# Kernel optimization log

Hardware: AMD Instinct MI355X
Metric: run time of the kernel (lower is better)

## Reference

```python
import jax, jax.numpy as jnp
import numpy as np
from jax import lax

BN_EPS = 1e-5
K_TOP = 2


def _conv_bn_relu_pool(x, w, b, g, beta, mean, var):
    # x: [B,C,H,W], w: [O,I,3,3]; SAME conv -> eval BN -> ReLU -> 2x2 maxpool
    y = lax.conv_general_dilated(x, w, (1, 1), 'SAME',
                                 dimension_numbers=('NCHW', 'OIHW', 'NCHW'))
    y = y + b[None, :, None, None]
    inv = g / jnp.sqrt(var + BN_EPS)
    y = (y - mean[None, :, None, None]) * inv[None, :, None, None] + beta[None, :, None, None]
    y = jax.nn.relu(y)
    return lax.reduce_window(y, -jnp.inf, lax.max, (1, 1, 2, 2), (1, 1, 2, 2), 'VALID')


def setup_inputs() -> dict:
    key = jax.random.key(0)
    ks = jax.random.split(key, 12)
    B, F_DIM, H_DIM, OUT, E = 4096, 128, 64, 10, 8
    d = {}
    d['x'] = jax.random.normal(ks[0], (B, 3, 32, 32), dtype=jnp.float32)
    # conv stacks
    def conv_block(k, cin, cout, i):
        kk = jax.random.split(k, 2)
        d[f'conv{i}_w'] = jax.random.normal(kk[0], (cout, cin, 3, 3), dtype=jnp.float32) * (1.0 / np.sqrt(cin * 9))
        d[f'conv{i}_b'] = jnp.zeros((cout,), dtype=jnp.float32)
        d[f'bn{i}_g'] = jnp.ones((cout,), dtype=jnp.float32)
        d[f'bn{i}_b'] = jnp.zeros((cout,), dtype=jnp.float32)
        d[f'bn{i}_m'] = jax.random.normal(kk[1], (cout,), dtype=jnp.float32) * 0.1
        d[f'bn{i}_v'] = jnp.ones((cout,), dtype=jnp.float32)
    conv_block(ks[1], 3, 32, 1)
    conv_block(ks[2], 32, 64, 2)
    conv_block(ks[3], 64, 128, 3)
    # experts (stacked): MLPHead Linear(128,64) -> ReLU -> Linear(64,10)
    d['w1'] = jax.random.normal(ks[4], (E, F_DIM, H_DIM), dtype=jnp.float32) * (1.0 / np.sqrt(F_DIM))
    d['b1'] = jnp.zeros((E, H_DIM), dtype=jnp.float32)
    d['w2'] = jax.random.normal(ks[5], (E, H_DIM, OUT), dtype=jnp.float32) * (1.0 / np.sqrt(H_DIM))
    d['b2'] = jnp.zeros((E, OUT), dtype=jnp.float32)
    # top-k gate: Linear(128, 8)
    d['gate_w'] = jax.random.normal(ks[6], (F_DIM, E), dtype=jnp.float32) * (1.0 / np.sqrt(F_DIM))
    d['gate_b'] = jnp.zeros((E,), dtype=jnp.float32)
    return d


def reference(x, conv1_w, conv1_b, bn1_g, bn1_b, bn1_m, bn1_v,
              conv2_w, conv2_b, bn2_g, bn2_b, bn2_m, bn2_v,
              conv3_w, conv3_b, bn3_g, bn3_b, bn3_m, bn3_v,
              w1, b1, w2, b2, gate_w, gate_b):
    # Backbone: 3x32x32 -> 128 (eval-mode BN, dropout identity)
    h = _conv_bn_relu_pool(x, conv1_w, conv1_b, bn1_g, bn1_b, bn1_m, bn1_v)  # [B,32,16,16]
    h = _conv_bn_relu_pool(h, conv2_w, conv2_b, bn2_g, bn2_b, bn2_m, bn2_v)  # [B,64,8,8]
    h = _conv_bn_relu_pool(h, conv3_w, conv3_b, bn3_g, bn3_b, bn3_m, bn3_v)  # [B,128,4,4]
    feat = jnp.mean(h, axis=(2, 3))  # AdaptiveAvgPool2d(1) + Flatten -> [B,128]

    # Top-k gate: logits -> top-k -> softmax over selected -> scatter to [B,E]
    logits = feat @ gate_w + gate_b                     # [B,E]
    vals, idx = lax.top_k(logits, K_TOP)                # [B,k]
    wk = jax.nn.softmax(vals, axis=-1)                  # [B,k]
    B, E = logits.shape
    weights = jnp.zeros((B, E), dtype=logits.dtype)
    weights = weights.at[jnp.arange(B)[:, None], idx].set(wk)

    # Dense expert MLPs (as in source), gate-weighted sum
    he = jax.nn.relu(jnp.einsum('bf,efh->beh', feat, w1) + b1[None])  # [B,E,H]
    oe = jnp.einsum('beh,eho->beo', he, w2) + b2[None]                # [B,E,O]
    return jnp.einsum('be,beo->bo', weights, oe)                      # [B,O]
```

## Files before the change

### kernel.cpp

```cpp
#include <hip/hip_runtime.h>
#include <math.h>

typedef __attribute__((ext_vector_type(8))) short short8;
typedef __attribute__((ext_vector_type(4))) float f32x4;
typedef __attribute__((ext_vector_type(16))) float f32x16;
#define MFMA16 __builtin_amdgcn_mfma_f32_16x16x32_bf16
#define MFMA32 __builtin_amdgcn_mfma_f32_32x32x16_bf16

#define BN_EPS 1e-5f

static const size_t W1C2_OFF = 0;
static const size_t W2C2_OFF = 1024;
static const size_t W3C2_OFF = 19456;
static const size_t B1_OFF   = 93184;
static const size_t B2_OFF   = 93216;
static const size_t B3_OFF   = 93280;

__device__ inline unsigned short rneb(float x) {
    unsigned u = __float_as_uint(x);
    return (unsigned short)((u + 0x7FFFu + ((u >> 16) & 1u)) >> 16);
}
__device__ inline float b2f(unsigned short h) {
    return __uint_as_float(((unsigned)h) << 16);
}

__global__ __launch_bounds__(256) void k_prep(
    const float* __restrict__ c1w, const float* __restrict__ c2w, const float* __restrict__ c3w,
    const float* __restrict__ c1b, const float* __restrict__ g1, const float* __restrict__ be1,
    const float* __restrict__ m1, const float* __restrict__ v1,
    const float* __restrict__ c2b, const float* __restrict__ g2, const float* __restrict__ be2,
    const float* __restrict__ m2, const float* __restrict__ v2,
    const float* __restrict__ c3b, const float* __restrict__ g3, const float* __restrict__ be3,
    const float* __restrict__ m3, const float* __restrict__ v3,
    unsigned short* __restrict__ w1c2, unsigned short* __restrict__ w2c2,
    unsigned short* __restrict__ w3c2,
    float* __restrict__ b1c, float* __restrict__ b2c, float* __restrict__ b3c)
{
    int i = blockIdx.x * 256 + threadIdx.x;
    if (i < 2048) {
        int e = i & 7, p = (i >> 3) & 1, kc = (i >> 4) & 3, ol = (i >> 6) & 15, n = i >> 10;
        int o = n * 16 + ol, k = kc * 8 + e;
        float s = g1[o] * rsqrtf(v1[o] + BN_EPS);
        float wv = (k < 27) ? c1w[o * 27 + k] * s : 0.f;
        unsigned short h = rneb(wv);
        w1c2[i] = p ? rneb(wv - b2f(h)) : h;
        return;
    }
    i -= 2048;
    if (i < 36864) {
        int e = i & 7, p = (i >> 3) & 1, kh = (i >> 4) & 1, col = (i >> 5) & 31;
        int nt = (i >> 10) & 1, ks = (i >> 11) & 1, tap = i >> 12;
        int o = nt * 32 + col, ci = ks * 16 + kh * 8 + e;
        float s = g2[o] * rsqrtf(v2[o] + BN_EPS);
        float wv = c2w[o * 288 + ci * 9 + tap] * s;
        unsigned short h = rneb(wv);
        w2c2[i] = p ? rneb(wv - b2f(h)) : h;
        return;
    }
    i -= 36864;
    if (i < 147456) {
        int e = i & 7, p = (i >> 3) & 1, kh = (i >> 4) & 1, col = (i >> 5) & 31;
        int nf = (i >> 10) & 3, ks = (i >> 12) & 3, tap = i >> 14;
        int o = nf * 32 + col, ci = ks * 16 + kh * 8 + e;
        float sc = g3[o] * rsqrtf(v3[o] + BN_EPS);
        float wv = c3w[o * 576 + ci * 9 + tap] * sc;
        unsigned short h = rneb(wv);
        w3c2[i] = p ? rneb(wv - b2f(h)) : h;
        return;
    }
    i -= 147456;
    if (i < 32) { float s = g1[i]*rsqrtf(v1[i]+BN_EPS); b1c[i] = (c1b[i]-m1[i])*s + be1[i]; return; }
    i -= 32;
    if (i < 64) { float s = g2[i]*rsqrtf(v2[i]+BN_EPS); b2c[i] = (c2b[i]-m2[i])*s + be2[i]; return; }
    i -= 64;
    if (i < 128) { float s = g3[i]*rsqrtf(v3[i]+BN_EPS); b3c[i] = (c3b[i]-m3[i])*s + be3[i]; return; }
}

__global__ __launch_bounds__(512, 4) void k_fused(
    const float* __restrict__ x,
    const unsigned short* __restrict__ w1c2,
    const unsigned short* __restrict__ w2c2,
    const unsigned short* __restrict__ w3c2,
    const float* __restrict__ b1c, const float* __restrict__ b2c, const float* __restrict__ b3c,
    const float* __restrict__ w1e, const float* __restrict__ b1e,
    const float* __restrict__ w2e, const float* __restrict__ b2e,
    const float* __restrict__ gw, const float* __restrict__ gb,
    float* __restrict__ out)
{
    __shared__ __align__(16) unsigned short R1[20736];
    __shared__ __align__(16) unsigned int   R2x[3074];
    float* sFeatP = (float*)R2x;
    float* sPart  = (float*)R2x + 256;
    float* sOutB  = (float*)R2x + 768;

    const int b = blockIdx.x, t = threadIdx.x;
    const int lane = t & 63, w = t >> 6;
    const int l15 = lane & 15, lg = lane >> 4;
    const int4 z4 = {0, 0, 0, 0};

    {
        const float* xb = x + (size_t)b * 3072;
        for (int i = t; i < 3072; i += 512) {
            float v = xb[i];
            unsigned short h = rneb(v);
            unsigned short lo = rneb(v - b2f(h));
            R2x[i] = ((unsigned)h << 16) | lo;
        }
        if (t == 0) R2x[3072] = 0;
        for (int hh = t; hh < 272; hh += 512) {
            int pr = hh >> 2, kc = hh & 3;
            int py, px;
            if (pr < 36) { py = (pr < 18) ? 0 : 17; px = (pr < 18) ? pr : pr - 18; }
            else { int r = pr - 36; py = 1 + (r >> 1); px = (r & 1) ? 17 : 0; }
            int ei = ((py * 4 + kc) * 18 + px) * 8;
            *(int4*)(R1 + ei) = z4;
            *(int4*)(R1 + 10368 + ei) = z4;
        }
    }
    __syncthreads();

    {
        short8 b1h[2], b1l[2];
#pragma unroll
        for (int n = 0; n < 2; n++) {
            const short8* bp = (const short8*)(w1c2 + 16 * ((n * 16 + l15) * 4 + lg));
            b1h[n] = bp[0]; b1l[n] = bp[1];
        }
        int dyE[8], dxE[8], cbE[8];
#pragma unroll
        for (int e = 0; e < 8; e++) {
            int k = lg * 8 + e;
            if (k < 27) { int ci = k / 9, tp = k - ci * 9;
                          dyE[e] = tp / 3 - 1; dxE[e] = tp % 3 - 1; cbE[e] = ci << 10; }
            else { dyE[e] = -1000; dxE[e] = 0; cbE[e] = 0; }
        }
        float bia[2] = { b1c[l15], b1c[16 + l15] };
#pragma unroll 1
        for (int q = 0; q < 2; q++) {
            int m0 = 8 * w + 4 * q;
            f32x4 acc[4][2];
#pragma unroll
            for (int mi = 0; mi < 4; mi++)
#pragma unroll
                for (int n = 0; n < 2; n++) acc[mi][n] = (f32x4)0.f;
#pragma unroll
            for (int mi = 0; mi < 4; mi++) {
                int pos = 16 * (m0 + mi) + l15, py = pos >> 5, px = pos & 31;
                short8 ah, al;
#pragma unroll
                for (int e = 0; e < 8; e++) {
                    int yy = py + dyE[e], xv = px + dxE[e];
                    int idx = cbE[e] + (yy << 5) + xv;
                    bool ok = ((unsigned)yy < 32u) && ((unsigned)xv < 32u);
                    unsigned u = R2x[ok ? idx : 3072];
                    ah[e] = (short)(u >> 16);
                    al[e] = (short)(u & 0xFFFFu);
                }
#pragma unroll
                for (int n = 0; n < 2; n++) {
                    acc[mi][n] = MFMA16(ah, b1h[n], acc[mi][n], 0, 0, 0);
                    acc[mi][n] = MFMA16(ah, b1l[n], acc[mi][n], 0, 0, 0);
                    acc[mi][n] = MFMA16(al, b1h[n], acc[mi][n], 0, 0, 0);
                }
            }
            int PY = 2 * w + q;
#pragma unroll
            for (int n = 0; n < 2; n++) {
                int o = n * 16 + l15;
#pragma unroll
                for (int h = 0; h < 2; h++)
#pragma unroll
                for (int jp = 0; jp < 2; jp++) {
                    float v00 = fmaxf(acc[h][n][2*jp]     + bia[n], 0.f);
                    float v01 = fmaxf(acc[h][n][2*jp + 1] + bia[n], 0.f);
                    float v10 = fmaxf(acc[h+2][n][2*jp]     + bia[n], 0.f);
                    float v11 = fmaxf(acc[h+2][n][2*jp + 1] + bia[n], 0.f);
                    float pm = fmaxf(fmaxf(v00, v01), fmaxf(v10, v11));
                    int PX = h * 8 + lg * 2 + jp;
                    unsigned short ph = rneb(pm), pl = rneb(pm - b2f(ph));
                    int ei = (((PY + 1) * 4 + (o >> 3)) * 18 + (PX + 1)) * 8 + (o & 7);
                    R1[ei] = ph; R1[10368 + ei] = pl;
                }
            }
        }
    }
    __syncthreads();

    {
        const int nt = w & 1, wm = w >> 1;
        const int r = lane & 31, kh = lane >> 5;
        f32x16 acc2A = (f32x16)0.f, acc2B = (f32x16)0.f;
        const unsigned short* wb = w2c2 + ((size_t)(nt * 32 + r) * 2 + kh) * 16;
        const int pyb0 = 2 * (2 * wm)     + (r >> 4);
        const int pyb1 = 2 * (2 * wm + 1) + (r >> 4);
        const int pxb = r & 15;
#pragma unroll
        for (int u = 0; u < 18; u++) {
            const int tap_ = u >> 1, ks_ = u & 1;
            const int dy_ = tap_ / 3, dx_ = tap_ - 3 * dy_;
            const int kc_ = ks_ * 2 + kh;
            const int co_ = (kc_ * 18 + pxb + dx_) * 8;
            const short8* bp = (const short8*)(wb + u * 2048);
            short8 bh = bp[0], bl = bp[1];
            {
                int ea_ = (pyb0 + dy_) * 576 + co_;
                short8 ah_ = *(const short8*)(R1 + ea_);
                short8 al_ = *(const short8*)(R1 + 10368 + ea_);
                acc2A = MFMA32(ah_, bh, acc2A, 0, 0, 0);
                acc2A = MFMA32(ah_, bl, acc2A, 0, 0, 0);
                acc2A = MFMA32(al_, bh, acc2A, 0, 0, 0);
            }
            {
                int ea_ = (pyb1 + dy_) * 576 + co_;
                short8 ah_ = *(const short8*)(R1 + ea_);
                short8 al_ = *(const short8*)(R1 + 10368 + ea_);
                acc2B = MFMA32(ah_, bh, acc2B, 0, 0, 0);
                acc2B = MFMA32(ah_, bl, acc2B, 0, 0, 0);
                acc2B = MFMA32(al_, bh, acc2B, 0, 0, 0);
            }
        }
        __syncthreads();
        for (int hh = t; hh < 288; hh += 512) {
            int pr = hh >> 3, kc = hh & 7;
            int py, px;
            if (pr < 20) { py = (pr < 10) ? 0 : 9; px = (pr < 10) ? pr : pr - 10; }
            else { int rr = pr - 20; py = 1 + (rr >> 1); px = (rr & 1) ? 9 : 0; }
            int ei = ((py * 8 + kc) * 11 + px) * 8;
            *(int4*)(R1 + ei) = z4;
            *(int4*)(R1 + 7040 + ei) = z4;
        }
        {
            int oc = nt * 32 + r;
            float bia = b2c[oc];
#define EPI2(ACC, MT) { \
            _Pragma("unroll") for (int g = 0; g < 4; g++) { \
                float v0 = fmaxf(ACC[2*g]     + bia, 0.f); \
                float v1 = fmaxf(ACC[2*g + 1] + bia, 0.f); \
                float v2 = fmaxf(ACC[2*g + 8] + bia, 0.f); \
                float v3 = fmaxf(ACC[2*g + 9] + bia, 0.f); \
                float pm = fmaxf(fmaxf(v0, v1), fmaxf(v2, v3)); \
                int PX = (g & 1) + (g >> 1) * 4 + kh * 2; \
                int ei = ((((MT) + 1) * 8 + (oc >> 3)) * 11 + (PX + 1)) * 8 + (oc & 7); \
                unsigned short ph = rneb(pm); \
                R1[ei] = ph; R1[7040 + ei] = rneb(pm - b2f(ph)); } }
            EPI2(acc2A, 2 * wm);
            EPI2(acc2B, 2 * wm + 1);
        }
    }
    __syncthreads();

    {
        const int mt = w >> 2, nf = w & 3;
        const int r = lane & 31, kh = lane >> 5;
        f32x16 acc3a = (f32x16)0.f, acc3b = (f32x16)0.f;
        const unsigned short* wb3 = w3c2 + ((size_t)(nf * 32 + r) * 2 + kh) * 16;
        const int pyb = mt * 4 + (r >> 3), pxb = r & 7;
#pragma unroll
        for (int u = 0; u < 36; u += 2) {
            {
                const int tap_ = u >> 2, ks_ = u & 3;
                const int dy_ = tap_ / 3, dx_ = tap_ - 3 * dy_;
                const int kc_ = ks_ * 2 + kh;
                int ea_ = (((pyb + dy_) * 8 + kc_) * 11 + (pxb + dx_)) * 8;
                const short8* bp = (const short8*)(wb3 + u * 4096);
                short8 bh = bp[0], bl = bp[1];
                short8 ah_ = *(const short8*)(R1 + ea_);
                short8 al_ = *(const short8*)(R1 + 7040 + ea_);
                acc3a = MFMA32(ah_, bh, acc3a, 0, 0, 0);
                acc3a = MFMA32(ah_, bl, acc3a, 0, 0, 0);
                acc3a = MFMA32(al_, bh, acc3a, 0, 0, 0);
            }
            {
                const int u1 = u + 1;
                const int tap_ = u1 >> 2, ks_ = u1 & 3;
                const int dy_ = tap_ / 3, dx_ = tap_ - 3 * dy_;
                const int kc_ = ks_ * 2 + kh;
                int ea_ = (((pyb + dy_) * 8 + kc_) * 11 + (pxb + dx_)) * 8;
                const short8* bp = (const short8*)(wb3 + u1 * 4096);
                short8 bh = bp[0], bl = bp[1];
                short8 ah_ = *(const short8*)(R1 + ea_);
                short8 al_ = *(const short8*)(R1 + 7040 + ea_);
                acc3b = MFMA32(ah_, bh, acc3b, 0, 0, 0);
                acc3b = MFMA32(ah_, bl, acc3b, 0, 0, 0);
                acc3b = MFMA32(al_, bh, acc3b, 0, 0, 0);
            }
        }
        {
            int oc = nf * 32 + r;
            float bia = b3c[oc];
            float fs = 0.f;
#pragma unroll
            for (int pl = 0; pl < 2; pl++)
#pragma unroll
            for (int g = 0; g < 2; g++) {
                float v0 = fmaxf(acc3a[pl*8 + 2*g]     + acc3b[pl*8 + 2*g]     + bia, 0.f);
                float v1 = fmaxf(acc3a[pl*8 + 2*g + 1] + acc3b[pl*8 + 2*g + 1] + bia, 0.f);
                float v2 = fmaxf(acc3a[pl*8 + 2*g + 4] + acc3b[pl*8 + 2*g + 4] + bia, 0.f);
                float v3 = fmaxf(acc3a[pl*8 + 2*g + 5] + acc3b[pl*8 + 2*g + 5] + bia, 0.f);
                fs += fmaxf(fmaxf(v0, v1), fmaxf(v2, v3));
            }
            fs += __shfl_xor(fs, 32, 64);
            if (lane < 32) sFeatP[mt * 128 + oc] = fs;
        }
    }
    __syncthreads();
    if (t < 128) sFeatP[t] = (sFeatP[t] + sFeatP[128 + t]) * (1.0f / 16.0f);
    __syncthreads();

    int i1 = 0, i2 = 0;
    float wk1 = 0.f, wk2 = 0.f;
    {
        float f0 = sFeatP[lane], f1 = sFeatP[64 + lane];
        float lgt[8];
#pragma unroll
        for (int e = 0; e < 8; e++) {
            float p = f0 * gw[lane * 8 + e] + f1 * gw[(64 + lane) * 8 + e];
#pragma unroll
            for (int s = 1; s < 64; s <<= 1) p += __shfl_xor(p, s, 64);
            lgt[e] = p + gb[e];
        }
        float v1m = -1e30f, v2m = -1e30f;
#pragma unroll
        for (int e = 0; e < 8; e++) {
            float le = lgt[e];
            if (le > v1m) { v2m = v1m; i2 = i1; v1m = le; i1 = e; }
            else if (le > v2m) { v2m = le; i2 = e; }
        }
        float ex = expf(v2m - v1m);
        wk1 = 1.f / (1.f + ex); wk2 = ex / (1.f + ex);
        int e = (w < 4) ? i1 : i2;
        int k0 = (w & 3) * 32;
        const float* W1 = w1e + (size_t)e * 8192 + (size_t)k0 * 64;
        float hj = 0.f;
#pragma unroll 8
        for (int kk = 0; kk < 32; kk++) hj += sFeatP[k0 + kk] * W1[kk * 64 + lane];
        sPart[w * 64 + lane] = hj;
    }
    __syncthreads();
    if (w < 2) {
        int e = (w == 0) ? i1 : i2;
        float wk = (w == 0) ? wk1 : wk2;
        float hj = b1e[e * 64 + lane]
                 + sPart[(w * 4 + 0) * 64 + lane] + sPart[(w * 4 + 1) * 64 + lane]
                 + sPart[(w * 4 + 2) * 64 + lane] + sPart[(w * 4 + 3) * 64 + lane];
        hj = fmaxf(hj, 0.f);
        const float* W2 = w2e + (size_t)e * 640 + lane * 10;
#pragma unroll
        for (int o = 0; o < 10; o++) {
            float po = hj * W2[o];
#pragma unroll
            for (int s = 1; s < 64; s <<= 1) po += __shfl_xor(po, s, 64);
            if (lane == 0) sOutB[w * 10 + o] = wk * (po + b2e[e * 10 + o]);
        }
    }
    __syncthreads();
    if (t < 10) out[(size_t)b * 10 + t] = sOutB[t] + sOutB[10 + t];
}

extern "C" void kernel_launch(void* const* d_in, const int* in_sizes, int n_in,
                              void* d_out, int out_size, void* d_ws, size_t ws_size,
                              hipStream_t stream)
{
    const float* x   = (const float*)d_in[0];
    const float* c1w = (const float*)d_in[1];
    const float* c1b = (const float*)d_in[2];
    const float* g1  = (const float*)d_in[3];
    const float* be1 = (const float*)d_in[4];
    const float* m1  = (const float*)d_in[5];
    const float* v1  = (const float*)d_in[6];
    const float* c2w = (const float*)d_in[7];
    const float* c2b = (const float*)d_in[8];
    const float* g2  = (const float*)d_in[9];
    const float* be2 = (const float*)d_in[10];
    const float* m2  = (const float*)d_in[11];
    const float* v2  = (const float*)d_in[12];
    const float* c3w = (const float*)d_in[13];
    const float* c3b = (const float*)d_in[14];
    const float* g3  = (const float*)d_in[15];
    const float* be3 = (const float*)d_in[16];
    const float* m3  = (const float*)d_in[17];
    const float* v3  = (const float*)d_in[18];
    const float* w1e = (const float*)d_in[19];
    const float* b1e = (const float*)d_in[20];
    const float* w2e = (const float*)d_in[21];
    const float* b2e = (const float*)d_in[22];
    const float* gw  = (const float*)d_in[23];
    const float* gb  = (const float*)d_in[24];

    float* ws = (float*)d_ws;
    unsigned short* w1c2 = (unsigned short*)(ws + W1C2_OFF);
    unsigned short* w2c2 = (unsigned short*)(ws + W2C2_OFF);
    unsigned short* w3c2 = (unsigned short*)(ws + W3C2_OFF);
    float* b1c = ws + B1_OFF;
    float* b2c = ws + B2_OFF;
    float* b3c = ws + B3_OFF;

    k_prep<<<729, 256, 0, stream>>>(c1w, c2w, c3w,
                                    c1b, g1, be1, m1, v1,
                                    c2b, g2, be2, m2, v2,
                                    c3b, g3, be3, m3, v3,
                                    w1c2, w2c2, w3c2, b1c, b2c, b3c);
    k_fused<<<4096, 512, 0, stream>>>(x, w1c2, w2c2, w3c2, b1c, b2c, b3c,
                                      w1e, b1e, w2e, b2e, gw, gb, (float*)d_out);
}
```

Before: 305.7 us.

## Pad input halo in LDS and reshape conv2/conv3 wave tiling for A-operand reuse

The conv1 input is now stored in LDS with a zero halo, so the im2col gather drops its per-element bounds checks and the sentinel slot. Conv2 waves now each cover one row tile across both 32-channel output halves, so each LDS A-fragment load feeds two accumulators. Conv3 splits the K loop between wave pairs, with each wave computing two output-channel tiles, and reduces the partial sums through LDS scratch. This cuts LDS A-operand traffic and address arithmetic. In exchange it adds a split-K reduction with extra barriers and more global weight loads per wave.

Result: slower. 347.1 us (+13.6%).

```diff
diff --git a/kernel.cpp b/kernel.cpp
--- a/kernel.cpp
+++ b/kernel.cpp
@@ -22,6 +22,10 @@
 }
 __device__ inline float b2f(unsigned short h) {
     return __uint_as_float(((unsigned)h) << 16);
+}
+__device__ inline unsigned packhl(float v) {
+    unsigned short h = rneb(v);
+    return ((unsigned)h << 16) | (unsigned)rneb(v - b2f(h));
 }
 
 __global__ __launch_bounds__(256) void k_prep(
@@ -88,10 +92,10 @@
     float* __restrict__ out)
 {
     __shared__ __align__(16) unsigned short R1[20736];
-    __shared__ __align__(16) unsigned int   R2x[3074];
-    float* sFeatP = (float*)R2x;
-    float* sPart  = (float*)R2x + 256;
-    float* sOutB  = (float*)R2x + 768;
+    __shared__ __align__(16) unsigned int   xs[3468];
+    float* sFeatP = (float*)xs;
+    float* sPart  = (float*)xs + 256;
+    float* sOutB  = (float*)xs + 768;
 
     const int b = blockIdx.x, t = threadIdx.x;
     const int lane = t & 63, w = t >> 6;
@@ -101,12 +105,17 @@
     {
         const float* xb = x + (size_t)b * 3072;
         for (int i = t; i < 3072; i += 512) {
-            float v = xb[i];
-            unsigned short h = rneb(v);
-            unsigned short lo = rneb(v - b2f(h));
-            R2x[i] = ((unsigned)h << 16) | lo;
-        }
-        if (t == 0) R2x[3072] = 0;
+            int ci = i >> 10, y = (i >> 5) & 31, xx = i & 31;
+            xs[ci * 1156 + (y + 1) * 34 + (xx + 1)] = packhl(xb[i]);
+        }
+        for (int hh = t; hh < 396; hh += 512) {
+            int ci = (hh * 31776) >> 22;
+            int r = hh - ci * 132;
+            int yy, xx;
+            if (r < 68) { yy = (r < 34) ? 0 : 33; xx = (r < 34) ? r : r - 34; }
+            else { int rr = r - 68; yy = 1 + (rr >> 1); xx = (rr & 1) ? 33 : 0; }
+            xs[ci * 1156 + yy * 34 + xx] = 0u;
+        }
         for (int hh = t; hh < 272; hh += 512) {
             int pr = hh >> 2, kc = hh & 3;
             int py, px;
@@ -126,13 +135,13 @@
             const short8* bp = (const short8*)(w1c2 + 16 * ((n * 16 + l15) * 4 + lg));
             b1h[n] = bp[0]; b1l[n] = bp[1];
         }
-        int dyE[8], dxE[8], cbE[8];
+        int aoffU[8];
 #pragma unroll
         for (int e = 0; e < 8; e++) {
             int k = lg * 8 + e;
             if (k < 27) { int ci = k / 9, tp = k - ci * 9;
-                          dyE[e] = tp / 3 - 1; dxE[e] = tp % 3 - 1; cbE[e] = ci << 10; }
-            else { dyE[e] = -1000; dxE[e] = 0; cbE[e] = 0; }
+                          aoffU[e] = ci * 1156 + (tp / 3) * 34 + (tp % 3); }
+            else aoffU[e] = 0;
         }
         float bia[2] = { b1c[l15], b1c[16 + l15] };
 #pragma unroll 1
@@ -146,13 +155,11 @@
 #pragma unroll
             for (int mi = 0; mi < 4; mi++) {
                 int pos = 16 * (m0 + mi) + l15, py = pos >> 5, px = pos & 31;
+                int base = py * 34 + px;
                 short8 ah, al;
 #pragma unroll
                 for (int e = 0; e < 8; e++) {
-                    int yy = py + dyE[e], xv = px + dxE[e];
-                    int idx = cbE[e] + (yy << 5) + xv;
-                    bool ok = ((unsigned)yy < 32u) && ((unsigned)xv < 32u);
-                    unsigned u = R2x[ok ? idx : 3072];
+                    unsigned u = xs[base + aoffU[e]];
                     ah[e] = (short)(u >> 16);
                     al[e] = (short)(u & 0xFFFFu);
                 }
@@ -187,37 +194,29 @@
     __syncthreads();
 
     {
-        const int nt = w & 1, wm = w >> 1;
         const int r = lane & 31, kh = lane >> 5;
         f32x16 acc2A = (f32x16)0.f, acc2B = (f32x16)0.f;
-        const unsigned short* wb = w2c2 + ((size_t)(nt * 32 + r) * 2 + kh) * 16;
-        const int pyb0 = 2 * (2 * wm)     + (r >> 4);
-        const int pyb1 = 2 * (2 * wm + 1) + (r >> 4);
+        const unsigned short* wb = w2c2 + (size_t)(r * 2 + kh) * 16;
+        const int pyb = 2 * w + (r >> 4);
         const int pxb = r & 15;
 #pragma unroll
         for (int u = 0; u < 18; u++) {
             const int tap_ = u >> 1, ks_ = u & 1;
             const int dy_ = tap_ / 3, dx_ = tap_ - 3 * dy_;
             const int kc_ = ks_ * 2 + kh;
-            const int co_ = (kc_ * 18 + pxb + dx_) * 8;
-            const short8* bp = (const short8*)(wb + u * 2048);
-            short8 bh = bp[0], bl = bp[1];
-            {
-                int ea_ = (pyb0 + dy_) * 576 + co_;
-                short8 ah_ = *(const short8*)(R1 + ea_);
-                short8 al_ = *(const short8*)(R1 + 10368 + ea_);
-                acc2A = MFMA32(ah_, bh, acc2A, 0, 0, 0);
-                acc2A = MFMA32(ah_, bl, acc2A, 0, 0, 0);
-                acc2A = MFMA32(al_, bh, acc2A, 0, 0, 0);
-            }
-            {
-                int ea_ = (pyb1 + dy_) * 576 + co_;
-                short8 ah_ = *(const short8*)(R1 + ea_);
-                short8 al_ = *(const short8*)(R1 + 10368 + ea_);
-                acc2B = MFMA32(ah_, bh, acc2B, 0, 0, 0);
-                acc2B = MFMA32(ah_, bl, acc2B, 0, 0, 0);
-                acc2B = MFMA32(al_, bh, acc2B, 0, 0, 0);
-            }
+            int ea_ = (pyb + dy_) * 576 + (kc_ * 18 + pxb + dx_) * 8;
+            short8 ah_ = *(const short8*)(R1 + ea_);
+            short8 al_ = *(const short8*)(R1 + 10368 + ea_);
+            const short8* bp0 = (const short8*)(wb + (u * 2 + 0) * 1024);
+            short8 b0h = bp0[0], b0l = bp0[1];
+            acc2A = MFMA32(ah_, b0h, acc2A, 0, 0, 0);
+            acc2A = MFMA32(ah_, b0l, acc2A, 0, 0, 0);
+            acc2A = MFMA32(al_, b0h, acc2A, 0, 0, 0);
+            const short8* bp1 = (const short8*)(wb + (u * 2 + 1) * 1024);
+            short8 b1h_ = bp1[0], b1l_ = bp1[1];
+            acc2B = MFMA32(ah_, b1h_, acc2B, 0, 0, 0);
+            acc2B = MFMA32(ah_, b1l_, acc2B, 0, 0, 0);
+            acc2B = MFMA32(al_, b1h_, acc2B, 0, 0, 0);
         }
         __syncthreads();
         for (int hh = t; hh < 288; hh += 512) {
@@ -230,9 +229,8 @@
             *(int4*)(R1 + 7040 + ei) = z4;
         }
         {
-            int oc = nt * 32 + r;
-            float bia = b2c[oc];
-#define EPI2(ACC, MT) { \
+#define EPI2(ACC, MT, OC) { \
+            float bia = b2c[OC]; \
             _Pragma("unroll") for (int g = 0; g < 4; g++) { \
                 float v0 = fmaxf(ACC[2*g]     + bia, 0.f); \
                 float v1 = fmaxf(ACC[2*g + 1] + bia, 0.f); \
@@ -240,67 +238,77 @@
                 float v3 = fmaxf(ACC[2*g + 9] + bia, 0.f); \
                 float pm = fmaxf(fmaxf(v0, v1), fmaxf(v2, v3)); \
                 int PX = (g & 1) + (g >> 1) * 4 + kh * 2; \
-                int ei = ((((MT) + 1) * 8 + (oc >> 3)) * 11 + (PX + 1)) * 8 + (oc & 7); \
+                int ei = ((((MT) + 1) * 8 + ((OC) >> 3)) * 11 + (PX + 1)) * 8 + ((OC) & 7); \
                 unsigned short ph = rneb(pm); \
                 R1[ei] = ph; R1[7040 + ei] = rneb(pm - b2f(ph)); } }
-            EPI2(acc2A, 2 * wm);
-            EPI2(acc2B, 2 * wm + 1);
+            EPI2(acc2A, w, r);
+            EPI2(acc2B, w, 32 + r);
         }
     }
     __syncthreads();
 
     {
-        const int mt = w >> 2, nf = w & 3;
+        const int mt = w >> 2, np = (w >> 1) & 1, kp = w & 1;
+        const int nf0 = np * 2;
         const int r = lane & 31, kh = lane >> 5;
-        f32x16 acc3a = (f32x16)0.f, acc3b = (f32x16)0.f;
-        const unsigned short* wb3 = w3c2 + ((size_t)(nf * 32 + r) * 2 + kh) * 16;
+        f32x16 accA = (f32x16)0.f, accB = (f32x16)0.f;
+        const unsigned short* wb3 = w3c2 + (size_t)(r * 2 + kh) * 16;
         const int pyb = mt * 4 + (r >> 3), pxb = r & 7;
-#pragma unroll
-        for (int u = 0; u < 36; u += 2) {
-            {
-                const int tap_ = u >> 2, ks_ = u & 3;
-                const int dy_ = tap_ / 3, dx_ = tap_ - 3 * dy_;
-                const int kc_ = ks_ * 2 + kh;
-                int ea_ = (((pyb + dy_) * 8 + kc_) * 11 + (pxb + dx_)) * 8;
-                const short8* bp = (const short8*)(wb3 + u * 4096);
-                short8 bh = bp[0], bl = bp[1];
-                short8 ah_ = *(const short8*)(R1 + ea_);
-                short8 al_ = *(const short8*)(R1 + 7040 + ea_);
-                acc3a = MFMA32(ah_, bh, acc3a, 0, 0, 0);
-                acc3a = MFMA32(ah_, bl, acc3a, 0, 0, 0);
-                acc3a = MFMA32(al_, bh, acc3a, 0, 0, 0);
-            }
-            {
-                const int u1 = u + 1;
-                const int tap_ = u1 >> 2, ks_ = u1 & 3;
-                const int dy_ = tap_ / 3, dx_ = tap_ - 3 * dy_;
-                const int kc_ = ks_ * 2 + kh;
-                int ea_ = (((pyb + dy_) * 8 + kc_) * 11 + (pxb + dx_)) * 8;
-                const short8* bp = (const short8*)(wb3 + u1 * 4096);
-                short8 bh = bp[0], bl = bp[1];
-                short8 ah_ = *(const short8*)(R1 + ea_);
-                short8 al_ = *(const short8*)(R1 + 7040 + ea_);
-                acc3b = MFMA32(ah_, bh, acc3b, 0, 0, 0);
-                acc3b = MFMA32(ah_, bl, acc3b, 0, 0, 0);
-                acc3b = MFMA32(al_, bh, acc3b, 0, 0, 0);
-            }
-        }
-        {
-            int oc = nf * 32 + r;
-            float bia = b3c[oc];
-            float fs = 0.f;
-#pragma unroll
-            for (int pl = 0; pl < 2; pl++)
-#pragma unroll
-            for (int g = 0; g < 2; g++) {
-                float v0 = fmaxf(acc3a[pl*8 + 2*g]     + acc3b[pl*8 + 2*g]     + bia, 0.f);
-                float v1 = fmaxf(acc3a[pl*8 + 2*g + 1] + acc3b[pl*8 + 2*g + 1] + bia, 0.f);
-                float v2 = fmaxf(acc3a[pl*8 + 2*g + 4] + acc3b[pl*8 + 2*g + 4] + bia, 0.f);
-                float v3 = fmaxf(acc3a[pl*8 + 2*g + 5] + acc3b[pl*8 + 2*g + 5] + bia, 0.f);
-                fs += fmaxf(fmaxf(v0, v1), fmaxf(v2, v3));
-            }
-            fs += __shfl_xor(fs, 32, 64);
-            if (lane < 32) sFeatP[mt * 128 + oc] = fs;
+#define P3STEP(u) { \
+        const int tap_ = (u) >> 2, ks_ = (u) & 3; \
+        const int dy_ = tap_ / 3, dx_ = tap_ - 3 * dy_; \
+        const int kc_ = ks_ * 2 + kh; \
+        int ea_ = (((pyb + dy_) * 8 + kc_) * 11 + (pxb + dx_)) * 8; \
+        short8 ah_ = *(const short8*)(R1 + ea_); \
+        short8 al_ = *(const short8*)(R1 + 7040 + ea_); \
+        const short8* bp0_ = (const short8*)(wb3 + ((u) * 4 + nf0) * 1024); \
+        short8 b0h_ = bp0_[0], b0l_ = bp0_[1]; \
+        accA = MFMA32(ah_, b0h_, accA, 0, 0, 0); \
+        accA = MFMA32(ah_, b0l_, accA, 0, 0, 0); \
+        accA = MFMA32(al_, b0h_, accA, 0, 0, 0); \
+        const short8* bp1_ = (const short8*)(wb3 + ((u) * 4 + nf0 + 1) * 1024); \
+        short8 b1h_ = bp1_[0], b1l_ = bp1_[1]; \
+        accB = MFMA32(ah_, b1h_, accB, 0, 0, 0); \
+        accB = MFMA32(ah_, b1l_, accB, 0, 0, 0); \
+        accB = MFMA32(al_, b1h_, accB, 0, 0, 0); }
+        if (kp == 0) {
+#pragma unroll
+            for (int u = 0; u < 18; u++) P3STEP(u)
+        } else {
+#pragma unroll
+            for (int u = 18; u < 36; u++) P3STEP(u)
+        }
+        __syncthreads();
+        float* scr = (float*)R1;
+        const int j = mt * 2 + np;
+        if (kp == 1) {
+            float* pA = scr + (size_t)((j * 2 + 0) * 64 + lane) * 16;
+            float* pB = scr + (size_t)((j * 2 + 1) * 64 + lane) * 16;
+#pragma unroll
+            for (int i2 = 0; i2 < 16; i2++) { pA[i2] = accA[i2]; pB[i2] = accB[i2]; }
+        }
+        __syncthreads();
+        if (kp == 0) {
+            float* pA = scr + (size_t)((j * 2 + 0) * 64 + lane) * 16;
+            float* pB = scr + (size_t)((j * 2 + 1) * 64 + lane) * 16;
+#pragma unroll
+            for (int i2 = 0; i2 < 16; i2++) { accA[i2] += pA[i2]; accB[i2] += pB[i2]; }
+#define EPI3(ACC, NF) { \
+            int oc = (NF) * 32 + r; \
+            float bia = b3c[oc]; \
+            float fs = 0.f; \
+            _Pragma("unroll") for (int pl = 0; pl < 2; pl++) \
+            _Pragma("unroll") for (int g = 0; g < 2; g++) { \
+                float v0 = fmaxf(ACC[pl*8 + 2*g]     + bia, 0.f); \
+                float v1 = fmaxf(ACC[pl*8 + 2*g + 1] + bia, 0.f); \
+                float v2 = fmaxf(ACC[pl*8 + 2*g + 4] + bia, 0.f); \
+                float v3 = fmaxf(ACC[pl*8 + 2*g + 5] + bia, 0.f); \
+                fs += fmaxf(fmaxf(v0, v1), fmaxf(v2, v3)); \
+            } \
+            fs += __shfl_xor(fs, 32, 64); \
+            if (lane < 32) sFeatP[mt * 128 + oc] = fs; }
+            EPI3(accA, nf0);
+            EPI3(accB, nf0 + 1);
         }
     }
     __syncthreads();
```
